# Kernel optimization log

Hardware: AMD Instinct MI355X
Metric: run time of the kernel (lower is better)

## Reference

```python
import jax, jax.numpy as jnp
from jax import lax
import numpy as np

IMG = 1024                      # image_size (square)
RPN_TRAIN_THRES = 0.5
RATIOS = jnp.array([0.5, 1.0, 2.0], jnp.float32)
SCALES = jnp.array([0.2, 0.4, 0.7], jnp.float32)
K_GT = 16


def _conv(x, w, b, stride):
    # NHWC x HWIO -> NHWC, VALID padding (keras Conv2D default)
    return lax.conv_general_dilated(x, w, (stride, stride), 'VALID',
                                    dimension_numbers=('NHWC', 'HWIO', 'NHWC')) + b


def _anchor_set():
    # [-w/2, -h/2, w/2, h/2] for 9 ratio/scale combos
    rs = jnp.sqrt(RATIOS)[:, None]                      # (3,1)
    ws = (SCALES[None, :] * rs).reshape(-1)             # (9,)
    hs = (SCALES[None, :] / rs).reshape(-1)
    return jnp.stack([ws, hs, ws, hs], axis=1) * 0.5 * jnp.array([-1.0, -1.0, 1.0, 1.0], jnp.float32)


def _anchors_pre(h, w):
    # mirrors generate_anchors_pre (incl. tf.transpose reversing axes -> (W,H,4));
    # feature map is square here so the layout matches the original.
    x = jnp.arange(0.0, 1.0, 1.0 / w, dtype=jnp.float32)
    y = jnp.arange(0.0, 1.0, 1.0 / h, dtype=jnp.float32)
    xx, yy = jnp.meshgrid(x, y)                         # (H,W)
    centers = jnp.stack([xx, yy, xx, yy], 0).transpose(2, 1, 0)  # (W,H,4)
    return centers[:, :, None, :] + _anchor_set()       # (W,H,9,4)


def _iou(b1, b2, gw, gh):
    gwh = jnp.array([gw, gh], jnp.float32)
    s1 = jnp.prod(b1[..., 2:] - b1[..., :2] + gwh, axis=-1)
    s2 = jnp.prod(b2[..., 2:] - b2[..., :2] + gwh, axis=-1)
    xa = jnp.maximum(b1[..., 0], b2[..., 0])
    ya = jnp.maximum(b1[..., 1], b2[..., 1])
    xb = jnp.minimum(b1[..., 2], b2[..., 2])
    yb = jnp.minimum(b1[..., 3], b2[..., 3])
    inter = jnp.maximum(xb - xa + gw, 0.0) * jnp.maximum(yb - ya + gh, 0.0)
    return inter / (s1 + s2 - inter)


def setup_inputs() -> dict:
    key = jax.random.key(0)
    ks = jax.random.split(key, 10)
    image = jax.random.uniform(ks[0], (1, IMG, IMG, 3), jnp.float32)
    cxy = jax.random.uniform(ks[1], (K_GT, 2), jnp.float32, 0.2, 0.8)
    wh = jax.random.uniform(ks[2], (K_GT, 2), jnp.float32, 0.1, 0.4)
    gt_boxes = jnp.concatenate([cxy - wh / 2, cxy + wh / 2], axis=1)  # (K,4) x1,y1,x2,y2
    Wb = jax.random.normal(ks[3], (4, 4, 3, 128), jnp.float32) * 0.05
    bb = jnp.zeros((128,), jnp.float32)
    Wi = jax.random.normal(ks[4], (3, 3, 128, 256), jnp.float32) * 0.05
    bi = jnp.zeros((256,), jnp.float32)
    Wc = jax.random.normal(ks[5], (1, 1, 256, 9), jnp.float32) * 0.05
    bc = jnp.zeros((9,), jnp.float32)
    Wr = jax.random.normal(ks[6], (1, 1, 256, 36), jnp.float32) * 0.05
    br = jnp.zeros((36,), jnp.float32)
    return {'image': image, 'gt_boxes': gt_boxes, 'Wb': Wb, 'bb': bb,
            'Wi': Wi, 'bi': bi, 'Wc': Wc, 'bc': bc, 'Wr': Wr, 'br': br}


def reference(image, gt_boxes, Wb, bb, Wi, bi, Wc, bc, Wr, br):
    feats = _conv(image, Wb, bb, 4)            # backbone: (1,256,256,128)
    fmap = _conv(feats, Wi, bi, 1)             # inter_conv: (1,254,254,256)
    fh, fw = fmap.shape[1], fmap.shape[2]
    gw = 1.0 / IMG
    gh = 1.0 / IMG
    anchors = _anchors_pre(fh, fw).reshape(-1, 4)          # (N,4), N = fh*fw*9
    inside = ((anchors[:, 0] >= 0.0) & (anchors[:, 1] >= 0.0) &
              (anchors[:, 2] < 1.0) & (anchors[:, 3] < 1.0))
    iou = _iou(anchors[:, None, :], gt_boxes[None, :, :], gw, gh)  # (N,K)
    max_iou = jnp.max(iou, axis=1)
    iou_in = jnp.where(inside[:, None], iou, -1.0)
    gt_max_iou = jnp.max(iou_in, axis=0)                   # (K,)
    is_gt_best = jnp.any((iou_in == gt_max_iou[None, :]) & inside[:, None], axis=1)
    pos = inside & (is_gt_best | (max_iou >= RPN_TRAIN_THRES))
    labels = jnp.where(inside, 0.0, -1.0)
    labels = jnp.where(pos, 1.0, labels)                   # (N,) in {-1,0,1}
    # RPN classification loss (BCE with logits) over labels != -1
    cls = _conv(fmap, Wc, bc, 1).reshape(-1)               # (N,)
    sel = (labels != -1.0).astype(jnp.float32)
    lbl = jnp.maximum(labels, 0.0)
    bce = lbl * jax.nn.softplus(-cls) + (1.0 - lbl) * jax.nn.softplus(cls)
    cls_loss = jnp.sum(bce * sel) / jnp.sum(sel)
    # smooth-L1 box loss, faithful to the original (it masks bbox_pred, not the diff)
    reg = _conv(fmap, Wr, br, 1).reshape(-1, 4)            # (N,4)
    m = pos.astype(jnp.float32)[:, None]                   # (N,1) bbox_mask
    ab = jnp.abs(reg * m)
    ss = (ab < 1.0).astype(jnp.float32)
    box_loss = ab * ab * 0.5 * ss + (ab - 0.5) * (1.0 - ss)
    bbox_loss = jnp.sum(box_loss) / jnp.sum(m)
    return cls_loss + bbox_loss
```

## Files before the change

kernel.cpp:

```cpp
#include <hip/hip_runtime.h>

#define F2      254
#define NPIX    (F2 * F2)
#define KGT     16
#define GWC     (1.0f / 1024.0f)

typedef __attribute__((ext_vector_type(8))) short bf16x8;
typedef __attribute__((ext_vector_type(4))) float f32x4;

__device__ unsigned short g_feats[16 * 65536 * 8];
__device__ unsigned short g_W2s[36 * 3 * 64 * 8];
__device__ float          g_b2[48];
__device__ float          g_acc[4] = {0.0f, 0.0f, 0.0f, 0.0f};
__device__ unsigned       g_keys[KGT] = {
    0x407FFFFFu, 0x407FFFFFu, 0x407FFFFFu, 0x407FFFFFu,
    0x407FFFFFu, 0x407FFFFFu, 0x407FFFFFu, 0x407FFFFFu,
    0x407FFFFFu, 0x407FFFFFu, 0x407FFFFFu, 0x407FFFFFu,
    0x407FFFFFu, 0x407FFFFFu, 0x407FFFFFu, 0x407FFFFFu};
__device__ unsigned       g_done = 0u;

__device__ __forceinline__ float b2f(unsigned short h) {
    return __uint_as_float(((unsigned)h) << 16);
}
__device__ __forceinline__ unsigned short f2b(float f) {
    unsigned u = __float_as_uint(f);
    unsigned r = (u + 0x7FFFu + ((u >> 16) & 1u)) >> 16;
    return (unsigned short)r;
}

__device__ __forceinline__ void iou16(float x1, float y1, float x2, float y2,
                                      const float* __restrict__ gt, float* __restrict__ v) {
    float s1 = (x2 - x1 + GWC) * (y2 - y1 + GWC);
#pragma unroll
    for (int k = 0; k < KGT; ++k) {
        float gx1 = gt[k * 4 + 0], gy1 = gt[k * 4 + 1];
        float gx2 = gt[k * 4 + 2], gy2 = gt[k * 4 + 3];
        float s2 = (gx2 - gx1 + GWC) * (gy2 - gy1 + GWC);
        float xa = fmaxf(x1, gx1), ya = fmaxf(y1, gy1);
        float xb = fminf(x2, gx2), yb = fminf(y2, gy2);
        float iw = fmaxf(xb - xa + GWC, 0.0f);
        float ih = fmaxf(yb - ya + GWC, 0.0f);
        float inter = iw * ih;
        v[k] = inter / (s1 + s2 - inter);
    }
}

__device__ __forceinline__ void type_extent(int a, float* hw, float* hh) {
    int ri = a / 3, si = a - ri * 3;
    float rat = (ri == 0) ? 0.5f : (ri == 1) ? 1.0f : 2.0f;
    float scl = (si == 0) ? 0.2f : (si == 1) ? 0.4f : 0.7f;
    float rs = sqrtf(rat);
    *hw = scl * rs * 0.5f;
    *hh = scl / rs * 0.5f;
}

__device__ __forceinline__ bf16x8 ld_a8(const float* ib, int kbase) {
    int r0 = kbase / 12, q0 = kbase - r0 * 12;
    unsigned short a8[8];
    float4 f0 = *(const float4*)(ib + (size_t)r0 * 3072 + q0);
    int k4 = kbase + 4;
    int r1 = k4 / 12, q1 = k4 - r1 * 12;
    float4 f1 = *(const float4*)(ib + (size_t)r1 * 3072 + q1);
    a8[0] = f2b(f0.x); a8[1] = f2b(f0.y); a8[2] = f2b(f0.z); a8[3] = f2b(f0.w);
    a8[4] = f2b(f1.x); a8[5] = f2b(f1.y); a8[6] = f2b(f1.z); a8[7] = f2b(f1.w);
    return *(bf16x8*)a8;
}

__global__ __launch_bounds__(256) void k_front(const float* __restrict__ img,
                                               const float* __restrict__ bb,
                                               const float* __restrict__ Wb,
                                               const float* __restrict__ Wi,
                                               const float* __restrict__ bi,
                                               const float* __restrict__ Wc,
                                               const float* __restrict__ bc,
                                               const float* __restrict__ Wr,
                                               const float* __restrict__ br,
                                               const float* __restrict__ gt) {
    __shared__ alignas(16) char sbuf[128 * 48 * 4];
    __shared__ float red[4][KGT];
    int t = threadIdx.x;
    int b = blockIdx.x;

    if (b < 1024) {
        unsigned short* wbs = (unsigned short*)sbuf;
#pragma unroll
        for (int it = 0; it < 4; ++it) {
            int e = t + it * 256;
            int kt = e >> 9, nt = (e >> 6) & 7, l = e & 63;
            unsigned short w8[8];
#pragma unroll
            for (int j = 0; j < 8; ++j) {
                int k = kt * 32 + ((l >> 4) * 8) + j;
                int oc = nt * 16 + (l & 15);
                w8[j] = (k < 48) ? f2b(Wb[(size_t)k * 128 + oc]) : (unsigned short)0;
            }
            *(ulonglong2*)(wbs + (size_t)e * 8) = *(ulonglong2*)w8;
        }
        __syncthreads();

        int cid = ((b & 7) << 7) + (b >> 3);
        int l = t & 63;
        int quad = l >> 4;
        int tile = cid * 4 + (t >> 6);
        int m0 = tile * 16;
        int p = m0 + (l & 15);
        int oy = p >> 8, ox = p & 255;
        const float* ib = img + ((size_t)oy * 4 * 1024 + (size_t)ox * 4) * 3;

        bf16x8 a0 = ld_a8(ib, quad * 8);
        bf16x8 a1 = (quad < 2) ? ld_a8(ib, 32 + quad * 8) : (bf16x8){0, 0, 0, 0, 0, 0, 0, 0};

        f32x4 acc[8];
#pragma unroll
        for (int nt = 0; nt < 8; ++nt) acc[nt] = (f32x4){0.0f, 0.0f, 0.0f, 0.0f};
#pragma unroll
        for (int nt = 0; nt < 8; ++nt) {
            bf16x8 b0 = *(const bf16x8*)(wbs + (size_t)(nt * 64 + l) * 8);
            bf16x8 b1 = *(const bf16x8*)(wbs + (size_t)((8 + nt) * 64 + l) * 8);
            acc[nt] = __builtin_amdgcn_mfma_f32_16x16x32_bf16(a0, b0, acc[nt], 0, 0, 0);
            acc[nt] = __builtin_amdgcn_mfma_f32_16x16x32_bf16(a1, b1, acc[nt], 0, 0, 0);
        }

        int n0 = l & 15;
        int mB = m0 + quad * 4;
#pragma unroll
        for (int nt = 0; nt < 8; ++nt) {
            int oc = nt * 16 + n0;
            float bias = bb[oc];
            int slab = oc >> 3;
            int ch = oc & 7;
#pragma unroll
            for (int r = 0; r < 4; ++r) {
                g_feats[((size_t)slab * 65536 + (mB + r)) * 8 + ch] = f2b(acc[nt][r] + bias);
            }
        }
        return;
    }

    if (b < 1312) {
        float (*wcr2)[48] = (float (*)[48])sbuf;
        int bw = b - 1024;
        int wave = __builtin_amdgcn_readfirstlane(t >> 6);
        int lane = t & 63;
        int k = bw * 4 + wave;
        int o = min(lane, 47);
        const float* wik = Wi + (size_t)k * 256;
        float acc = 0.0f;
        bool bias_thr = (b == 1024) && (t < 48);
        float a2 = 0.0f;
        if (bias_thr) a2 = (t < 9) ? bc[t] : ((t < 45) ? br[t - 9] : 0.0f);

        for (int pss = 0; pss < 2; ++pss) {
            __syncthreads();
            int ocb = pss * 128;
            for (int i = t; i < 1152; i += 256) {
                int oc = i / 9;
                wcr2[oc][i % 9] = Wc[(size_t)(ocb + oc) * 9 + i % 9];
            }
            for (int i = t; i < 4608; i += 256) {
                int oc = i / 36;
                wcr2[oc][9 + i % 36] = Wr[(size_t)(ocb + oc) * 36 + i % 36];
            }
            for (int i = t; i < 384; i += 256) wcr2[i / 3][45 + i % 3] = 0.0f;
            __syncthreads();
#pragma unroll 8
            for (int oc = 0; oc < 128; ++oc)
                acc = fmaf(wik[ocb + oc], wcr2[oc][o], acc);
            if (bias_thr) {
                for (int oc = 0; oc < 128; ++oc)
                    a2 = fmaf(bi[ocb + oc], wcr2[oc][t], a2);
            }
        }

        if (lane < 48) {
            int kt = k >> 5, r5 = k & 31, j = r5 & 7, lhi = r5 >> 3;
            int nt = o >> 4, llo = o & 15, l2 = lhi * 16 + llo;
            g_W2s[(size_t)((kt * 3 + nt) * 64 + l2) * 8 + j] = f2b(acc);
        }
        if (bias_thr) g_b2[t] = a2;
        return;
    }

    {
        int bid = b - 1312;
        int a = bid >> 5;
        int blk = bid & 31;
        float hw, hh;
        type_extent(a, &hw, &hh);
        float m16[KGT];
#pragma unroll
        for (int k = 0; k < KGT; ++k) m16[k] = -1.0f;
        for (int pix = blk * 256 + t; pix < NPIX; pix += 32 * 256) {
            int w = pix / F2, h = pix - w * F2;
            float cx = (float)w * (1.0f / 254.0f);
            float cy = (float)h * (1.0f / 254.0f);
            float x1 = cx - hw, y1 = cy - hh, x2 = cx + hw, y2 = cy + hh;
            bool inside = (x1 >= 0.0f) && (y1 >= 0.0f) && (x2 < 1.0f) && (y2 < 1.0f);
            if (__ballot(inside) == 0ull) continue;
            if (inside) {
                float v[KGT];
                iou16(x1, y1, x2, y2, gt, v);
#pragma unroll
                for (int k = 0; k < KGT; ++k) m16[k] = fmaxf(m16[k], v[k]);
            }
        }
#pragma unroll
        for (int k = 0; k < KGT; ++k) {
#pragma unroll
            for (int m = 32; m; m >>= 1) m16[k] = fmaxf(m16[k], __shfl_xor(m16[k], m, 64));
        }
        int lane = t & 63, wv = t >> 6;
        if (lane == 0) {
#pragma unroll
            for (int k = 0; k < KGT; ++k) red[wv][k] = m16[k];
        }
        __syncthreads();
        if (t < KGT) {
            float mx = fmaxf(fmaxf(red[0][t], red[1][t]), fmaxf(red[2][t], red[3][t]));
            unsigned u = __float_as_uint(mx);
            unsigned key = (u & 0x80000000u) ? ~u : (u | 0x80000000u);
            atomicMax(&g_keys[t], key);
        }
    }
}

__global__ __launch_bounds__(256) void k_convC_loss(const float* __restrict__ gt,
                                                    unsigned* __restrict__ out) {
    __shared__ alignas(16) unsigned short Bs[12 * 1536];
    __shared__ float redl[4][4];
    int t = threadIdx.x;
    int b = blockIdx.x;
    int xcd = b & 7;
    int cid = (xcd == 0) ? (b >> 3) : (64 + (xcd - 1) * 63 + (b >> 3));
    int l = t & 63;
    int quad = l >> 4;
    int wv = t >> 6;
    int tile = cid * 4 + wv;
    int m0 = tile * 32;
    int mA0 = min(m0 + (l & 15), NPIX - 1);
    int mA1 = min(m0 + 16 + (l & 15), NPIX - 1);
    int py0 = mA0 / F2, px0 = mA0 - py0 * F2;
    int py1 = mA1 / F2, px1 = mA1 - py1 * F2;

    f32x4 acc[2][3];
#pragma unroll
    for (int h = 0; h < 2; ++h)
#pragma unroll
        for (int nt = 0; nt < 3; ++nt) acc[h][nt] = (f32x4){0.0f, 0.0f, 0.0f, 0.0f};

    for (int c = 0; c < 3; ++c) {
        __syncthreads();
        {
            const uint4* src = (const uint4*)(g_W2s + (size_t)c * 18432);
            uint4* dst = (uint4*)Bs;
#pragma unroll
            for (int j = 0; j < 9; ++j) dst[t + 256 * j] = src[t + 256 * j];
        }
        __syncthreads();
#pragma unroll
        for (int i = 0; i < 12; ++i) {
            int kt = c * 12 + i;
            int pos = kt >> 2, kc = kt & 3;
            int ky = pos / 3, kx = pos - ky * 3;
            int slab = kc * 4 + quad;
            const unsigned short* ap0 =
                g_feats + ((size_t)slab * 65536 + ((py0 + ky) * 256 + (px0 + kx))) * 8;
            const unsigned short* ap1 =
                g_feats + ((size_t)slab * 65536 + ((py1 + ky) * 256 + (px1 + kx))) * 8;
            bf16x8 a0 = *(const bf16x8*)ap0;
            bf16x8 a1 = *(const bf16x8*)ap1;
            const unsigned short* bp = Bs + (size_t)i * 1536 + l * 8;
            bf16x8 b0 = *(const bf16x8*)(bp);
            bf16x8 b1 = *(const bf16x8*)(bp + 512);
            bf16x8 b2v = *(const bf16x8*)(bp + 1024);
            acc[0][0] = __builtin_amdgcn_mfma_f32_16x16x32_bf16(a0, b0, acc[0][0], 0, 0, 0);
            acc[0][1] = __builtin_amdgcn_mfma_f32_16x16x32_bf16(a0, b1, acc[0][1], 0, 0, 0);
            acc[0][2] = __builtin_amdgcn_mfma_f32_16x16x32_bf16(a0, b2v, acc[0][2], 0, 0, 0);
            acc[1][0] = __builtin_amdgcn_mfma_f32_16x16x32_bf16(a1, b0, acc[1][0], 0, 0, 0);
            acc[1][1] = __builtin_amdgcn_mfma_f32_16x16x32_bf16(a1, b1, acc[1][1], 0, 0, 0);
            acc[1][2] = __builtin_amdgcn_mfma_f32_16x16x32_bf16(a1, b2v, acc[1][2], 0, 0, 0);
        }
    }

    __syncthreads();
    float (*S)[129] = (float (*)[129])(void*)Bs;
    int n0 = l & 15;
#pragma unroll
    for (int h = 0; h < 2; ++h) {
        int plB = wv * 32 + h * 16 + quad * 4;
#pragma unroll
        for (int nt = 0; nt < 3; ++nt) {
            int n = nt * 16 + n0;
            float bias = g_b2[n];
#pragma unroll
            for (int r = 0; r < 4; ++r) S[n][plB + r] = acc[h][nt][r] + bias;
        }
    }
    __syncthreads();

    int m0b = cid * 128;
    float sb = 0.0f, ss = 0.0f, sx = 0.0f, sp = 0.0f;
    for (int idx = t; idx < 1152; idx += 256) {
        int a = idx >> 7;
        int pl = idx & 127;
        int m = m0b + pl;
        float hw, hhf;
        type_extent(a, &hw, &hhf);
        bool inside = false;
        float x1 = 0.0f, y1 = 0.0f, x2 = 0.0f, y2 = 0.0f;
        if (m < NPIX) {
            int pw = m / F2, ph = m - pw * F2;
            float cx = (float)pw * (1.0f / 254.0f);
            float cy = (float)ph * (1.0f / 254.0f);
            x1 = cx - hw; y1 = cy - hhf; x2 = cx + hw; y2 = cy + hhf;
            inside = (x1 >= 0.0f) && (y1 >= 0.0f) && (x2 < 1.0f) && (y2 < 1.0f);
        }
        if (__ballot(inside) == 0ull) continue;
        if (inside) {
            float v[KGT];
            iou16(x1, y1, x2, y2, gt, v);
            float maxi = -1.0f;
            bool best = false;
#pragma unroll
            for (int k = 0; k < KGT; ++k) {
                maxi = fmaxf(maxi, v[k]);
                unsigned e = g_keys[k];
                float gm = __uint_as_float((e & 0x80000000u) ? (e & 0x7FFFFFFFu) : ~e);
                best = best || (v[k] == gm);
            }
            bool ispos = best || (maxi >= 0.5f);
            float c = b2f(f2b(S[a][pl]));
            float z = ispos ? -c : c;
            sb += fmaxf(z, 0.0f) + log1pf(expf(-fabsf(z)));
            ss += 1.0f;
            if (ispos) {
                float aa;
                aa = fabsf(b2f(f2b(S[9 + 4 * a + 0][pl]))); sx += (aa < 1.0f) ? 0.5f * aa * aa : aa - 0.5f;
                aa = fabsf(b2f(f2b(S[9 + 4 * a + 1][pl]))); sx += (aa < 1.0f) ? 0.5f * aa * aa : aa - 0.5f;
                aa = fabsf(b2f(f2b(S[9 + 4 * a + 2][pl]))); sx += (aa < 1.0f) ? 0.5f * aa * aa : aa - 0.5f;
                aa = fabsf(b2f(f2b(S[9 + 4 * a + 3][pl]))); sx += (aa < 1.0f) ? 0.5f * aa * aa : aa - 0.5f;
                sp += 1.0f;
            }
        }
    }

#pragma unroll
    for (int mm = 32; mm; mm >>= 1) {
        sb += __shfl_xor(sb, mm, 64);
        ss += __shfl_xor(ss, mm, 64);
        sx += __shfl_xor(sx, mm, 64);
        sp += __shfl_xor(sp, mm, 64);
    }
    int lane = t & 63;
    if (lane == 0) { redl[wv][0] = sb; redl[wv][1] = ss; redl[wv][2] = sx; redl[wv][3] = sp; }
    __syncthreads();
    if (t < 4) {
        float s = redl[0][t] + redl[1][t] + redl[2][t] + redl[3][t];
        atomicAdd(&g_acc[t], s);
    }
    __syncthreads();
    if (t == 0) {
        unsigned prev = atomicAdd(&g_done, 1u);
        if (prev == 504u) {
            float a0 = atomicAdd(&g_acc[0], 0.0f);
            float a1 = atomicAdd(&g_acc[1], 0.0f);
            float a2 = atomicAdd(&g_acc[2], 0.0f);
            float a3 = atomicAdd(&g_acc[3], 0.0f);
            float res = a0 / a1 + a2 / a3;
            unsigned lo = (unsigned)f2b(res);
            unsigned hi = __float_as_uint(res) >> 16;
            out[0] = (hi << 16) | lo;
            g_acc[0] = 0.0f; g_acc[1] = 0.0f; g_acc[2] = 0.0f; g_acc[3] = 0.0f;
#pragma unroll
            for (int k = 0; k < KGT; ++k) g_keys[k] = 0x407FFFFFu;
            g_done = 0u;
        }
    }
}

extern "C" void kernel_launch(void* const* d_in, const int* in_sizes, int n_in,
                              void* d_out, int out_size, void* d_ws, size_t ws_size,
                              hipStream_t stream) {
    (void)in_sizes; (void)n_in; (void)out_size; (void)d_ws; (void)ws_size;
    const float* image = (const float*)d_in[0];
    const float* gt    = (const float*)d_in[1];
    const float* Wb    = (const float*)d_in[2];
    const float* bb    = (const float*)d_in[3];
    const float* Wi    = (const float*)d_in[4];
    const float* bi    = (const float*)d_in[5];
    const float* Wc    = (const float*)d_in[6];
    const float* bc    = (const float*)d_in[7];
    const float* Wr    = (const float*)d_in[8];
    const float* br    = (const float*)d_in[9];

    k_front     <<<1600, 256, 0, stream>>>(image, bb, Wb, Wi, bi, Wc, bc, Wr, br, gt);
    k_convC_loss<<<505, 256, 0, stream>>>(gt, (unsigned*)d_out);
}
```

Measured before the change: 124.4 us.

## Bound per-anchor IoU scan to inside region and spread atomics across slots

The GT-max IoU blocks now iterate only over the rectangular range of anchor centers that can lie inside the image for each anchor type, using 24 blocks per type instead of 32. Atomics for the GT max keys and the loss accumulators are spread over partitioned slots, so fewer blocks contend on each address. The final block sums the slots and the consumer kernel reads the keys once into shared memory. This removes wasted work on outside anchors and atomic serialization, but adds a reduction over the partitions and a new initial-state convention (zeroed keys), which depends on the first run starting from zero-initialized globals.

New measurement: 131.5 us. 5.7% more time.

```diff
diff --git a/kernel.cpp b/kernel.cpp
--- a/kernel.cpp
+++ b/kernel.cpp
@@ -11,12 +11,8 @@
 __device__ unsigned short g_feats[16 * 65536 * 8];
 __device__ unsigned short g_W2s[36 * 3 * 64 * 8];
 __device__ float          g_b2[48];
-__device__ float          g_acc[4] = {0.0f, 0.0f, 0.0f, 0.0f};
-__device__ unsigned       g_keys[KGT] = {
-    0x407FFFFFu, 0x407FFFFFu, 0x407FFFFFu, 0x407FFFFFu,
-    0x407FFFFFu, 0x407FFFFFu, 0x407FFFFFu, 0x407FFFFFu,
-    0x407FFFFFu, 0x407FFFFFu, 0x407FFFFFu, 0x407FFFFFu,
-    0x407FFFFFu, 0x407FFFFFu, 0x407FFFFFu, 0x407FFFFFu};
+__device__ float          g_accP[64][16];
+__device__ unsigned       g_keysP[24][16];
 __device__ unsigned       g_done = 0u;
 
 __device__ __forceinline__ float b2f(unsigned short h) {
@@ -182,21 +178,28 @@
     }
 
     {
-        int bid = b - 1312;
-        int a = bid >> 5;
-        int blk = bid & 31;
+        int unit = b - 1312;
+        int a = unit / 24;
+        int sub = unit % 24;
         float hw, hh;
         type_extent(a, &hw, &hh);
+        int wa0 = (int)floorf(254.0f * hw) - 1; if (wa0 < 0) wa0 = 0;
+        int wa1 = (int)ceilf(254.0f * (1.0f - hw)) + 1; if (wa1 > 253) wa1 = 253;
+        int ha0 = (int)floorf(254.0f * hh) - 1; if (ha0 < 0) ha0 = 0;
+        int ha1 = (int)ceilf(254.0f * (1.0f - hh)) + 1; if (ha1 > 253) ha1 = 253;
+        int wspan = wa1 - wa0 + 1, hspan = ha1 - ha0 + 1;
+        int N = wspan * hspan;
+
         float m16[KGT];
 #pragma unroll
         for (int k = 0; k < KGT; ++k) m16[k] = -1.0f;
-        for (int pix = blk * 256 + t; pix < NPIX; pix += 32 * 256) {
-            int w = pix / F2, h = pix - w * F2;
+        for (int idx = sub * 256 + t; idx < N; idx += 24 * 256) {
+            int w = wa0 + idx / hspan;
+            int h = ha0 + idx % hspan;
             float cx = (float)w * (1.0f / 254.0f);
             float cy = (float)h * (1.0f / 254.0f);
             float x1 = cx - hw, y1 = cy - hh, x2 = cx + hw, y2 = cy + hh;
             bool inside = (x1 >= 0.0f) && (y1 >= 0.0f) && (x2 < 1.0f) && (y2 < 1.0f);
-            if (__ballot(inside) == 0ull) continue;
             if (inside) {
                 float v[KGT];
                 iou16(x1, y1, x2, y2, gt, v);
@@ -219,7 +222,7 @@
             float mx = fmaxf(fmaxf(red[0][t], red[1][t]), fmaxf(red[2][t], red[3][t]));
             unsigned u = __float_as_uint(mx);
             unsigned key = (u & 0x80000000u) ? ~u : (u | 0x80000000u);
-            atomicMax(&g_keys[t], key);
+            atomicMax(&g_keysP[sub][t], key);
         }
     }
 }
@@ -228,6 +231,7 @@
                                                     unsigned* __restrict__ out) {
     __shared__ alignas(16) unsigned short Bs[12 * 1536];
     __shared__ float redl[4][4];
+    __shared__ float gmS[KGT];
     int t = threadIdx.x;
     int b = blockIdx.x;
     int xcd = b & 7;
@@ -296,6 +300,15 @@
             for (int r = 0; r < 4; ++r) S[n][plB + r] = acc[h][nt][r] + bias;
         }
     }
+    if (t < KGT) {
+        unsigned e = 0u;
+#pragma unroll
+        for (int r = 0; r < 24; ++r) {
+            unsigned v2 = g_keysP[r][t];
+            e = (v2 > e) ? v2 : e;
+        }
+        gmS[t] = __uint_as_float((e & 0x80000000u) ? (e & 0x7FFFFFFFu) : ~e);
+    }
     __syncthreads();
 
     int m0b = cid * 128;
@@ -324,9 +337,7 @@
 #pragma unroll
             for (int k = 0; k < KGT; ++k) {
                 maxi = fmaxf(maxi, v[k]);
-                unsigned e = g_keys[k];
-                float gm = __uint_as_float((e & 0x80000000u) ? (e & 0x7FFFFFFFu) : ~e);
-                best = best || (v[k] == gm);
+                best = best || (v[k] == gmS[k]);
             }
             bool ispos = best || (maxi >= 0.5f);
             float c = b2f(f2b(S[a][pl]));
@@ -356,23 +367,30 @@
     __syncthreads();
     if (t < 4) {
         float s = redl[0][t] + redl[1][t] + redl[2][t] + redl[3][t];
-        atomicAdd(&g_acc[t], s);
+        atomicAdd(&g_accP[b & 63][t], s);
     }
     __syncthreads();
     if (t == 0) {
         unsigned prev = atomicAdd(&g_done, 1u);
         if (prev == 504u) {
-            float a0 = atomicAdd(&g_acc[0], 0.0f);
-            float a1 = atomicAdd(&g_acc[1], 0.0f);
-            float a2 = atomicAdd(&g_acc[2], 0.0f);
-            float a3 = atomicAdd(&g_acc[3], 0.0f);
+            float a0 = 0.0f, a1 = 0.0f, a2 = 0.0f, a3 = 0.0f;
+            for (int r = 0; r < 64; ++r) {
+                a0 += __hip_atomic_load(&g_accP[r][0], __ATOMIC_RELAXED, __HIP_MEMORY_SCOPE_AGENT);
+                a1 += __hip_atomic_load(&g_accP[r][1], __ATOMIC_RELAXED, __HIP_MEMORY_SCOPE_AGENT);
+                a2 += __hip_atomic_load(&g_accP[r][2], __ATOMIC_RELAXED, __HIP_MEMORY_SCOPE_AGENT);
+                a3 += __hip_atomic_load(&g_accP[r][3], __ATOMIC_RELAXED, __HIP_MEMORY_SCOPE_AGENT);
+            }
             float res = a0 / a1 + a2 / a3;
             unsigned lo = (unsigned)f2b(res);
             unsigned hi = __float_as_uint(res) >> 16;
             out[0] = (hi << 16) | lo;
-            g_acc[0] = 0.0f; g_acc[1] = 0.0f; g_acc[2] = 0.0f; g_acc[3] = 0.0f;
-#pragma unroll
-            for (int k = 0; k < KGT; ++k) g_keys[k] = 0x407FFFFFu;
+            for (int r = 0; r < 64; ++r) {
+                g_accP[r][0] = 0.0f; g_accP[r][1] = 0.0f;
+                g_accP[r][2] = 0.0f; g_accP[r][3] = 0.0f;
+            }
+            for (int r = 0; r < 24; ++r)
+#pragma unroll
+                for (int k = 0; k < KGT; ++k) g_keysP[r][k] = 0u;
             g_done = 0u;
         }
     }
@@ -393,6 +411,6 @@
     const float* Wr    = (const float*)d_in[8];
     const float* br    = (const float*)d_in[9];
 
-    k_front     <<<1600, 256, 0, stream>>>(image, bb, Wb, Wi, bi, Wc, bc, Wr, br, gt);
+    k_front     <<<1528, 256, 0, stream>>>(image, bb, Wb, Wi, bi, Wc, bc, Wr, br, gt);
     k_convC_loss<<<505, 256, 0, stream>>>(gt, (unsigned*)d_out);
 }
```
